# Kernel optimization log

Hardware: AMD Instinct MI355X
Metric: run time of the kernel (lower is better)

Reference implementation:

```python
import jax, jax.numpy as jnp
import numpy as np


def setup_inputs() -> dict:
    key = jax.random.key(0)
    k1, k2 = jax.random.split(key)
    B, H, V, N = 256, 4096, 1024, 32
    v = jax.random.uniform(k1, (B, V, N), dtype=jnp.float32)
    W = jax.random.normal(k2, (H, V, N), dtype=jnp.float32) / np.sqrt(V * N + 2)
    b_h = jnp.zeros((H,), dtype=jnp.float32)
    b_v = jnp.zeros((V, N), dtype=jnp.float32)
    return {"v": v, "W": W, "b_h": b_h, "b_v": b_v}


def reference(v, W, b_h, b_v):
    # (v.unsqueeze(-3) * W).sum([-1,-2]) is a contraction over (visible, category):
    # einsum 'bvn,hvn->bh' — a GEMM with K = n_visible * n.
    logits = jnp.einsum('bvn,hvn->bh', v, W) + b_h          # [B, H]
    sp = jax.nn.softplus(logits).sum(-1)                     # [B]
    vt = jnp.einsum('bvn,vn->b', v, b_v)                     # [B]
    return sp + vt
```

## Files before the change

### kernel.cpp

```cpp
#include <hip/hip_runtime.h>
#include <hip/hip_bf16.h>
#include <stdint.h>

#define B_ 256
#define H_ 4096
#define K_ 32768

typedef __attribute__((ext_vector_type(8))) short bf16x8;
typedef __attribute__((ext_vector_type(4))) float f32x4;

__device__ __forceinline__ unsigned short f2bf(float x) {
    union { float f; unsigned int u; } c; c.f = x;
    unsigned int r = c.u + 0x7FFFu + ((c.u >> 16) & 1u);
    return (unsigned short)(r >> 16);
}

__device__ __forceinline__ short bfc(float x) {
    __hip_bfloat16 h = __float2bfloat16(x);
    union { __hip_bfloat16 h; short s; } c; c.h = h;
    return c.s;
}

__device__ __forceinline__ float softplus_f(float x) {
    return fmaxf(x, 0.0f) + log1pf(expf(-fabsf(x)));
}

__global__ __launch_bounds__(256) void prep_kernel(
    const float* __restrict__ v, const float* __restrict__ bv,
    __hip_bfloat16* __restrict__ vbf, float* __restrict__ vt)
{
    const int b = blockIdx.x;
    const int t = threadIdx.x;
    const float* vr = v + (size_t)b * K_;
    unsigned short* dr = (unsigned short*)(vbf + (size_t)b * K_);
    float acc = 0.f;
    for (int i = t * 8; i < K_; i += 256 * 8) {
        float4 x0 = *(const float4*)(vr + i);
        float4 x1 = *(const float4*)(vr + i + 4);
        float4 b0 = *(const float4*)(bv + i);
        float4 b1 = *(const float4*)(bv + i + 4);
        acc += x0.x*b0.x + x0.y*b0.y + x0.z*b0.z + x0.w*b0.w
             + x1.x*b1.x + x1.y*b1.y + x1.z*b1.z + x1.w*b1.w;
        ushort4 u0, u1;
        u0.x = f2bf(x0.x); u0.y = f2bf(x0.y); u0.z = f2bf(x0.z); u0.w = f2bf(x0.w);
        u1.x = f2bf(x1.x); u1.y = f2bf(x1.y); u1.z = f2bf(x1.z); u1.w = f2bf(x1.w);
        *(ushort4*)(dr + i)     = u0;
        *(ushort4*)(dr + i + 4) = u1;
    }
    __shared__ float sm[256];
    sm[t] = acc;
    __syncthreads();
    for (int s = 128; s > 0; s >>= 1) {
        if (t < s) sm[t] += sm[t + s];
        __syncthreads();
    }
    if (t == 0) vt[b] = sm[0];
}


#define NCONS 8
#define VMW(N)  asm volatile("s_waitcnt vmcnt(" #N ")" ::: "memory")
#define PBAR()  asm volatile("s_waitcnt lgkmcnt(0)\n\ts_barrier" ::: "memory")
#define CBAR()  asm volatile("s_barrier" ::: "memory")

#define P_ISS(BUF, TT, CC) do {                                                        \
    const float* p_ = wlb + (size_t)((CC) >> 2) * (16 * (size_t)K_)                    \
                          + (size_t)(TT) * 256 + ((CC) & 3) * 64;                      \
    BUF[0] = *(const float4*)p_;                                                       \
    BUF[1] = *(const float4*)(p_ + 4);                                                 \
    } while (0)

#define P_WR(BUF, SLOT_, CC) do {                                                      \
    int r_ = (((CC) >> 2) & 7) * 16 + rsub;                                            \
    int g_ = ((((CC) & 3) * 8 + l8) ^ r7);                                             \
    bf16x8 u_;                                                                         \
    u_[0]=bfc(BUF[0].x); u_[1]=bfc(BUF[0].y); u_[2]=bfc(BUF[0].z); u_[3]=bfc(BUF[0].w);\
    u_[4]=bfc(BUF[1].x); u_[5]=bfc(BUF[1].y); u_[6]=bfc(BUF[1].z); u_[7]=bfc(BUF[1].w);\
    *(bf16x8*)&wtile[(SLOT_) + r_ * 256 + g_ * 8] = u_;                                \
    } while (0)

__global__ __launch_bounds__(640, 4) void gemm_kernel(
    const __hip_bfloat16* __restrict__ vbf,
    const float* __restrict__ W,
    float* __restrict__ part,
    int KS, int NT)
{
    __shared__ __align__(16) unsigned short wtile[2 * 128 * 256];

    const int tid  = threadIdx.x;
    const int wid  = tid >> 6;
    const int lane = tid & 63;
    const int lr   = lane & 15;
    const int lg   = lane >> 4;

    const int bid   = blockIdx.x;
    const int sidx  = bid % KS;
    const int ht    = bid / KS;
    const int h0    = ht * 128;
    const int kbase = sidx * (NT * 256);

    if (wid < NCONS) {
        const __hip_bfloat16* ap0 = vbf + (size_t)(wid * 32 + lr) * K_ + kbase + lg * 8;
        const __hip_bfloat16* ap1 = ap0 + (size_t)16 * K_;

        f32x4 acc[2][8];
        #pragma unroll
        for (int m = 0; m < 2; ++m)
            #pragma unroll
            for (int n = 0; n < 8; ++n)
                acc[m][n] = (f32x4)(0.0f);

        CBAR();

        for (int t = 0; t < NT; ++t) {
            const unsigned short* wb = &wtile[(t & 1) * 32768];
            const size_t koff = (size_t)t * 256;
            #pragma unroll
            for (int s = 0; s < 8; ++s) {
                bf16x8 a0 = *(const bf16x8*)(ap0 + koff + s * 32);
                bf16x8 a1 = *(const bf16x8*)(ap1 + koff + s * 32);
                #pragma unroll
                for (int q = 0; q < 2; ++q) {
                    bf16x8 bfr[4];
                    #pragma unroll
                    for (int n = 0; n < 4; ++n) {
                        int row = (q * 4 + n) * 16 + lr;
                        int g   = (s * 4 + lg) ^ (lr & 7);
                        bfr[n] = *(const bf16x8*)&wb[row * 256 + g * 8];
                    }
                    #pragma unroll
                    for (int n = 0; n < 4; ++n) {
                        acc[0][q*4+n] = __builtin_amdgcn_mfma_f32_16x16x32_bf16(
                            a0, bfr[n], acc[0][q*4+n], 0, 0, 0);
                        acc[1][q*4+n] = __builtin_amdgcn_mfma_f32_16x16x32_bf16(
                            a1, bfr[n], acc[1][q*4+n], 0, 0, 0);
                    }
                }
            }
            CBAR();
        }

        float* pout = part + (size_t)sidx * ((size_t)B_ * H_) + h0;
        #pragma unroll
        for (int m = 0; m < 2; ++m)
            #pragma unroll
            for (int n = 0; n < 8; ++n)
                #pragma unroll
                for (int j = 0; j < 4; ++j) {
                    int brow = wid * 32 + m * 16 + lg * 4 + j;
                    int hcol = n * 16 + lr;
                    pout[(size_t)brow * H_ + hcol] = acc[m][n][j];
                }
    } else {
        const int gl   = (wid - NCONS) * 64 + lane;
        const int rsub = gl >> 3;
        const int l8   = gl & 7;
        const int r7   = rsub & 7;
        const float* wlb = W + (size_t)(h0 + rsub) * K_ + kbase + l8 * 8;

        float4 buf0[2], buf1[2], buf2[2], buf3[2];

        P_ISS(buf0, 0, 0); P_ISS(buf1, 0, 1); P_ISS(buf2, 0, 2); P_ISS(buf3, 0, 3);

        #pragma unroll
        for (int c = 0; c < 32; ++c) {
            VMW(6);
            if ((c & 3) == 0) { P_WR(buf0, 0, c); if (c < 28) P_ISS(buf0, 0, c+4); else P_ISS(buf0, 1, c-28); }
            if ((c & 3) == 1) { P_WR(buf1, 0, c); if (c < 28) P_ISS(buf1, 0, c+4); else P_ISS(buf1, 1, c-28); }
            if ((c & 3) == 2) { P_WR(buf2, 0, c); if (c < 28) P_ISS(buf2, 0, c+4); else P_ISS(buf2, 1, c-28); }
            if ((c & 3) == 3) { P_WR(buf3, 0, c); if (c < 28) P_ISS(buf3, 0, c+4); else P_ISS(buf3, 1, c-28); }
        }
        PBAR();

        for (int t = 0; t < NT - 2; ++t) {
            const int slot = ((t + 1) & 1) * 32768;
            #pragma unroll
            for (int c = 0; c < 32; ++c) {
                VMW(6);
                if ((c & 3) == 0) { P_WR(buf0, slot, c); if (c < 28) P_ISS(buf0, t+1, c+4); else P_ISS(buf0, t+2, c-28); }
                if ((c & 3) == 1) { P_WR(buf1, slot, c); if (c < 28) P_ISS(buf1, t+1, c+4); else P_ISS(buf1, t+2, c-28); }
                if ((c & 3) == 2) { P_WR(buf2, slot, c); if (c < 28) P_ISS(buf2, t+1, c+4); else P_ISS(buf2, t+2, c-28); }
                if ((c & 3) == 3) { P_WR(buf3, slot, c); if (c < 28) P_ISS(buf3, t+1, c+4); else P_ISS(buf3, t+2, c-28); }
            }
            PBAR();
        }

        {
            const int slot = ((NT - 1) & 1) * 32768;
            #pragma unroll
            for (int c = 0; c < 28; ++c) {
                VMW(6);
                if ((c & 3) == 0) { P_WR(buf0, slot, c); P_ISS(buf0, NT-1, c+4); }
                if ((c & 3) == 1) { P_WR(buf1, slot, c); P_ISS(buf1, NT-1, c+4); }
                if ((c & 3) == 2) { P_WR(buf2, slot, c); P_ISS(buf2, NT-1, c+4); }
                if ((c & 3) == 3) { P_WR(buf3, slot, c); P_ISS(buf3, NT-1, c+4); }
            }
            VMW(6); P_WR(buf0, slot, 28);
            VMW(4); P_WR(buf1, slot, 29);
            VMW(2); P_WR(buf2, slot, 30);
            VMW(0); P_WR(buf3, slot, 31);
            PBAR();
        }
        PBAR();
    }
}

__global__ __launch_bounds__(256) void reduce_kernel(
    const float* __restrict__ part, const float* __restrict__ bh,
    const float* __restrict__ vt, float* __restrict__ out, int KS)
{
    const int b = blockIdx.x;
    const int t = threadIdx.x;
    float sp = 0.f;
    const float* pb = part + (size_t)b * H_;
    for (int h = t * 4; h < H_; h += 256 * 4) {
        float4 l = *(const float4*)(bh + h);
        for (int s = 0; s < KS; ++s) {
            float4 p = *(const float4*)(pb + (size_t)s * B_ * H_ + h);
            l.x += p.x; l.y += p.y; l.z += p.z; l.w += p.w;
        }
        sp += softplus_f(l.x) + softplus_f(l.y) + softplus_f(l.z) + softplus_f(l.w);
    }
    __shared__ float sm[256];
    sm[t] = sp;
    __syncthreads();
    for (int r = 128; r > 0; r >>= 1) {
        if (t < r) sm[t] += sm[t + r];
        __syncthreads();
    }
    if (t == 0) out[b] = sm[0] + vt[b];
}

extern "C" void kernel_launch(void* const* d_in, const int* in_sizes, int n_in,
                              void* d_out, int out_size, void* d_ws, size_t ws_size,
                              hipStream_t stream)
{
    const float* v  = (const float*)d_in[0];
    const float* W  = (const float*)d_in[1];
    const float* bh = (const float*)d_in[2];
    const float* bv = (const float*)d_in[3];
    float* out = (float*)d_out;

    char* ws = (char*)d_ws;
    const size_t vbf_bytes = (size_t)B_ * K_ * sizeof(__hip_bfloat16);
    __hip_bfloat16* vbf = (__hip_bfloat16*)ws;

    int KS = 16;
    while (KS > 1 && vbf_bytes + (size_t)KS * B_ * H_ * 4 + 1024 > ws_size) KS >>= 1;

    float* part = (float*)(ws + vbf_bytes);
    float* vt   = (float*)(ws + vbf_bytes + (size_t)KS * B_ * H_ * 4);

    prep_kernel<<<B_, 256, 0, stream>>>(v, bv, vbf, vt);
    const int NT = (K_ / KS) / 256;
    gemm_kernel<<<(H_ / 128) * KS, 640, 0, stream>>>(vbf, W, part, KS, NT);
    reduce_kernel<<<B_, 256, 0, stream>>>(part, bh, vt, out, KS);
}
```

Before: 221.1 us.

## Restructure producer W loads to row-contiguous float4 with 16-way LDS swizzle

The producer waves now each own 64 rows of the W tile and load one float4 per lane per row, so a wave reads a contiguous 1 KB span of each row instead of scattered 32-byte chunks. Eight loads are kept in flight with an 8-deep register ring, and the conversion writes short4 chunks into LDS using an XOR swizzle over 16 groups. The consumer's B-fragment read swizzle changes to match. This should improve global load coalescing and reduce LDS bank conflicts, at the cost of more, smaller LDS stores and a different pipeline prologue and epilogue.

```diff
diff --git a/kernel.cpp b/kernel.cpp
--- a/kernel.cpp
+++ b/kernel.cpp
@@ -63,20 +63,20 @@
 #define PBAR()  asm volatile("s_waitcnt lgkmcnt(0)\n\ts_barrier" ::: "memory")
 #define CBAR()  asm volatile("s_barrier" ::: "memory")
 
-#define P_ISS(BUF, TT, CC) do {                                                        \
-    const float* p_ = wlb + (size_t)((CC) >> 2) * (16 * (size_t)K_)                    \
-                          + (size_t)(TT) * 256 + ((CC) & 3) * 64;                      \
-    BUF[0] = *(const float4*)p_;                                                       \
-    BUF[1] = *(const float4*)(p_ + 4);                                                 \
+#define PLD(BUF, TT, II) \
+    BUF = *(const float4*)(wsrc0 + (size_t)(II) * K_ + (size_t)(TT) * 256)
+
+#define PST(BUF, SLOT_, II) do {                                                       \
+    short4 u_;                                                                         \
+    u_.x = bfc(BUF.x); u_.y = bfc(BUF.y); u_.z = bfc(BUF.z); u_.w = bfc(BUF.w);        \
+    *(short4*)&wtile[(SLOT_) + (r0 + (II)) * 256 +                                     \
+                     (((lane >> 1) ^ ((II) & 15)) * 8) + ((lane & 1) * 4)] = u_;       \
     } while (0)
 
-#define P_WR(BUF, SLOT_, CC) do {                                                      \
-    int r_ = (((CC) >> 2) & 7) * 16 + rsub;                                            \
-    int g_ = ((((CC) & 3) * 8 + l8) ^ r7);                                             \
-    bf16x8 u_;                                                                         \
-    u_[0]=bfc(BUF[0].x); u_[1]=bfc(BUF[0].y); u_[2]=bfc(BUF[0].z); u_[3]=bfc(BUF[0].w);\
-    u_[4]=bfc(BUF[1].x); u_[5]=bfc(BUF[1].y); u_[6]=bfc(BUF[1].z); u_[7]=bfc(BUF[1].w);\
-    *(bf16x8*)&wtile[(SLOT_) + r_ * 256 + g_ * 8] = u_;                                \
+#define STEP(BUF, II, NTT, NII) do {                                                   \
+    VMW(7);                                                                            \
+    PST(BUF, slot, II);                                                                \
+    PLD(BUF, NTT, NII);                                                                \
     } while (0)
 
 __global__ __launch_bounds__(640, 4) void gemm_kernel(
@@ -125,7 +125,7 @@
                     #pragma unroll
                     for (int n = 0; n < 4; ++n) {
                         int row = (q * 4 + n) * 16 + lr;
-                        int g   = (s * 4 + lg) ^ (lr & 7);
+                        int g   = (s * 4 + lg) ^ lr;
                         bfr[n] = *(const bf16x8*)&wb[row * 256 + g * 8];
                     }
                     #pragma unroll
@@ -152,53 +152,39 @@
                     pout[(size_t)brow * H_ + hcol] = acc[m][n][j];
                 }
     } else {
-        const int gl   = (wid - NCONS) * 64 + lane;
-        const int rsub = gl >> 3;
-        const int l8   = gl & 7;
-        const int r7   = rsub & 7;
-        const float* wlb = W + (size_t)(h0 + rsub) * K_ + kbase + l8 * 8;
-
-        float4 buf0[2], buf1[2], buf2[2], buf3[2];
-
-        P_ISS(buf0, 0, 0); P_ISS(buf1, 0, 1); P_ISS(buf2, 0, 2); P_ISS(buf3, 0, 3);
-
-        #pragma unroll
-        for (int c = 0; c < 32; ++c) {
-            VMW(6);
-            if ((c & 3) == 0) { P_WR(buf0, 0, c); if (c < 28) P_ISS(buf0, 0, c+4); else P_ISS(buf0, 1, c-28); }
-            if ((c & 3) == 1) { P_WR(buf1, 0, c); if (c < 28) P_ISS(buf1, 0, c+4); else P_ISS(buf1, 1, c-28); }
-            if ((c & 3) == 2) { P_WR(buf2, 0, c); if (c < 28) P_ISS(buf2, 0, c+4); else P_ISS(buf2, 1, c-28); }
-            if ((c & 3) == 3) { P_WR(buf3, 0, c); if (c < 28) P_ISS(buf3, 0, c+4); else P_ISS(buf3, 1, c-28); }
-        }
-        PBAR();
-
-        for (int t = 0; t < NT - 2; ++t) {
-            const int slot = ((t + 1) & 1) * 32768;
-            #pragma unroll
-            for (int c = 0; c < 32; ++c) {
-                VMW(6);
-                if ((c & 3) == 0) { P_WR(buf0, slot, c); if (c < 28) P_ISS(buf0, t+1, c+4); else P_ISS(buf0, t+2, c-28); }
-                if ((c & 3) == 1) { P_WR(buf1, slot, c); if (c < 28) P_ISS(buf1, t+1, c+4); else P_ISS(buf1, t+2, c-28); }
-                if ((c & 3) == 2) { P_WR(buf2, slot, c); if (c < 28) P_ISS(buf2, t+1, c+4); else P_ISS(buf2, t+2, c-28); }
-                if ((c & 3) == 3) { P_WR(buf3, slot, c); if (c < 28) P_ISS(buf3, t+1, c+4); else P_ISS(buf3, t+2, c-28); }
+        const int pw = wid - NCONS;
+        const int r0 = pw * 64;
+        const float* wsrc0 = W + (size_t)(h0 + r0) * K_ + kbase + lane * 4;
+
+        float4 b0, b1, b2, b3, b4, b5, b6, b7;
+
+        PLD(b0, 0, 0); PLD(b1, 0, 1); PLD(b2, 0, 2); PLD(b3, 0, 3);
+        PLD(b4, 0, 4); PLD(b5, 0, 5); PLD(b6, 0, 6); PLD(b7, 0, 7);
+
+        for (int T = 0; T < NT; ++T) {
+            const int slot = (T & 1) * 32768;
+            #pragma unroll
+            for (int i0 = 0; i0 < 56; i0 += 8) {
+                STEP(b0, i0 + 0, T, i0 +  8); STEP(b1, i0 + 1, T, i0 +  9);
+                STEP(b2, i0 + 2, T, i0 + 10); STEP(b3, i0 + 3, T, i0 + 11);
+                STEP(b4, i0 + 4, T, i0 + 12); STEP(b5, i0 + 5, T, i0 + 13);
+                STEP(b6, i0 + 6, T, i0 + 14); STEP(b7, i0 + 7, T, i0 + 15);
             }
-            PBAR();
-        }
-
-        {
-            const int slot = ((NT - 1) & 1) * 32768;
-            #pragma unroll
-            for (int c = 0; c < 28; ++c) {
-                VMW(6);
-                if ((c & 3) == 0) { P_WR(buf0, slot, c); P_ISS(buf0, NT-1, c+4); }
-                if ((c & 3) == 1) { P_WR(buf1, slot, c); P_ISS(buf1, NT-1, c+4); }
-                if ((c & 3) == 2) { P_WR(buf2, slot, c); P_ISS(buf2, NT-1, c+4); }
-                if ((c & 3) == 3) { P_WR(buf3, slot, c); P_ISS(buf3, NT-1, c+4); }
+            if (T + 1 < NT) {
+                STEP(b0, 56, T + 1, 0); STEP(b1, 57, T + 1, 1);
+                STEP(b2, 58, T + 1, 2); STEP(b3, 59, T + 1, 3);
+                STEP(b4, 60, T + 1, 4); STEP(b5, 61, T + 1, 5);
+                STEP(b6, 62, T + 1, 6); STEP(b7, 63, T + 1, 7);
+            } else {
+                VMW(7); PST(b0, slot, 56);
+                VMW(6); PST(b1, slot, 57);
+                VMW(5); PST(b2, slot, 58);
+                VMW(4); PST(b3, slot, 59);
+                VMW(3); PST(b4, slot, 60);
+                VMW(2); PST(b5, slot, 61);
+                VMW(1); PST(b6, slot, 62);
+                VMW(0); PST(b7, slot, 63);
             }
-            VMW(6); P_WR(buf0, slot, 28);
-            VMW(4); P_WR(buf1, slot, 29);
-            VMW(2); P_WR(buf2, slot, 30);
-            VMW(0); P_WR(buf3, slot, 31);
             PBAR();
         }
         PBAR();
```

Result: slower. 381.6 us (+72.6%).
